# Kernel optimization log

Measured on AMD Instinct MI355X. Metric: run time of the kernel, lower is better.

## Reference

```python
import jax, jax.numpy as jnp
import numpy as np
from jax import lax

B, MIN, DIN = 16, 8, 16
MOUT, DOUT = 8, 16
H, W = 32, 32
K, S, P, OP = 3, 2, 1, 1
NH, NW = 64, 64
ITERS = 2
EPS = 1e-7


def squash(s):
    # s: [..., D]; matches torch squash: factor * s / safe_norm
    sq = jnp.sum(s * s, axis=-1, keepdims=True)
    norm = jnp.sqrt(sq + EPS)
    return (sq / (1.0 + sq)) * s / norm


def setup_inputs() -> dict:
    key = jax.random.key(0)
    k1, k2, k3 = jax.random.split(key, 3)
    x = jax.random.normal(k1, (B, MIN, H, W, DIN), dtype=jnp.float32)
    # torch ConvTranspose2d weight layout: [in_ch, out_ch, kH, kW]
    w_deconv = jax.random.normal(k2, (MIN * DIN, MOUT * DOUT, K, K), dtype=jnp.float32) * 0.05
    b_deconv = jax.random.normal(k3, (MOUT * DOUT,), dtype=jnp.float32) * 0.05
    b_route = jnp.zeros((1, MOUT, NH, NW, MIN), dtype=jnp.float32)
    return {"x": x, "w_deconv": w_deconv, "b_deconv": b_deconv, "b_route": b_route}


def reference(x, w_deconv, b_deconv, b_route):
    Bb, Min, Hh, Ww, Din = x.shape
    # [B, Min, H, W, Din] -> [B, Min*Din, H, W]
    xc = jnp.transpose(x, (0, 1, 4, 2, 3)).reshape(Bb, Min * Din, Hh, Ww)
    # ConvTranspose2d == conv with lhs_dilation=stride and spatially-flipped, IO-swapped kernel
    wf = jnp.transpose(w_deconv, (1, 0, 2, 3))[:, :, ::-1, ::-1]  # [out, in, kH, kW]
    pad = (K - 1 - P, K - 1 - P + OP)
    y = lax.conv_general_dilated(
        xc, wf, window_strides=(1, 1), padding=[pad, pad],
        lhs_dilation=(S, S), dimension_numbers=("NCHW", "OIHW", "NCHW"))
    y = y + b_deconv[None, :, None, None]  # [B, Mout*Dout, NH, NW]
    nh, nw = y.shape[2], y.shape[3]
    # view([B, Mout, Dout, h, w, -1]).permute(0,1,3,4,5,2) -> [B, Mout, h, w, 1, Dout]
    pred = jnp.transpose(y.reshape(Bb, MOUT, DOUT, nh, nw, 1), (0, 1, 3, 4, 5, 2))
    # --- agreement routing ---
    c = jax.nn.softmax(b_route, axis=-1)                      # [1, Mout, h, w, Min]
    out = squash(jnp.sum(c[..., None] * pred, axis=-2))       # [B, Mout, h, w, Dout]
    b = b_route
    for _ in range(ITERS):
        b = b + jnp.sum(pred * out[..., None, :], axis=-1)    # [B, Mout, h, w, Min]
        c = jax.nn.softmax(b, axis=-1)
        out = squash(jnp.sum(pred * c[..., None], axis=-2))
    return out
```

## Files before the change

kernel.cpp:

```cpp
#include <hip/hip_runtime.h>
#include <hip/hip_bf16.h>
#include <math.h>


typedef __attribute__((ext_vector_type(8))) __bf16 bf16x8;
typedef __attribute__((ext_vector_type(4))) float f32x4;

#define XBF_ELEMS (16 * 8 * 32 * 32 * 16)

__global__ __launch_bounds__(256) void prep(const float* __restrict__ x,
                                            const float* __restrict__ w,
                                            __hip_bfloat16* __restrict__ xbf,
                                            __hip_bfloat16* __restrict__ wl) {
    const int bx = blockIdx.x;
    if (bx < 1024) {
        const int i = (bx * 256 + threadIdx.x) * 8;
        float4 a = *(const float4*)(x + i);
        float4 b = *(const float4*)(x + i + 4);
        union { bf16x8 v; __hip_bfloat162 h[4]; } u;
        u.h[0] = __float22bfloat162_rn(make_float2(a.x, a.y));
        u.h[1] = __float22bfloat162_rn(make_float2(a.z, a.w));
        u.h[2] = __float22bfloat162_rn(make_float2(b.x, b.y));
        u.h[3] = __float22bfloat162_rn(make_float2(b.z, b.w));
        *(bf16x8*)(xbf + i) = u.v;
    } else {
        const int idx = (bx - 1024) * 256 + threadIdx.x;
        const int ci  = idx / 1152;
        const int rem = idx - ci * 1152;
        const int co  = rem / 9;
        const int tap = rem - co * 9;
        const int s = ci >> 5, quad = (ci >> 3) & 3, j = ci & 7;
        const int t = co >> 4, n16 = co & 15;
        const int dst = ((((tap * 4 + s) * 8 + t) * 64) + quad * 16 + n16) * 8 + j;
        wl[dst] = __float2bfloat16(w[idx]);
    }
}

template <int CTRL>
__device__ __forceinline__ float dpp_xadd(float v) {
    int p = __builtin_amdgcn_update_dpp(0, __float_as_int(v), CTRL, 0xF, 0xF, true);
    return v + __int_as_float(p);
}
__device__ __forceinline__ float rowsum16(float v) {
    v = dpp_xadd<0xB1>(v);
    v = dpp_xadd<0x4E>(v);
    v = dpp_xadd<0x141>(v);
    v = dpp_xadd<0x140>(v);
    return v;
}

template <int PH, int PW, int NT>
__device__ __forceinline__ void caps_body(
    const __hip_bfloat16* __restrict__ xbf, const __hip_bfloat16* __restrict__ wl,
    const float* __restrict__ bias, float* __restrict__ out,
    __hip_bfloat16* bsh, int t0)
{
    constexpr int NH = PH ? 2 : 1, NW = PW ? 2 : 1;
    constexpr int CHE = NT * 512;
    const int tid = threadIdx.x, lane = tid & 63, wv = tid >> 6;
    const int q = blockIdx.y, b = blockIdx.z;

    #pragma unroll
    for (int it = 0; it < 8; ++it) {
        const int idx    = it * 2048 + tid * 8;
        const int c2     = idx / CHE;
        const int within = idx % CHE;
        const int s  = c2 & 3, ti = c2 >> 2;
        const int kh = PH ? (ti / NW) * 2 : 1;
        const int kw = PW ? (ti % NW) * 2 : 1;
        const int tap = kh * 3 + kw;
        *(bf16x8*)(bsh + idx) =
            *(const bf16x8*)(wl + ((tap * 4 + s) * 8 + t0) * 512 + within);
    }
    __syncthreads();

    const int rp = wv >> 1, chf = wv & 1;
    const int rw0 = q * 4 + rp * 2;
    const int n16  = lane & 15;
    const int quad = lane >> 4;
    const int c    = chf * 16 + n16;

    float bb[NT];
    #pragma unroll
    for (int tt = 0; tt < NT; ++tt) bb[tt] = bias[(t0 + tt) * 16 + n16];

    const __hip_bfloat16* xq = xbf + b * 131072 + (quad >> 1) * 16384 + (quad & 1) * 8;

    f32x4 acc[2][NT];
    #pragma unroll
    for (int r = 0; r < 2; ++r)
        #pragma unroll
        for (int tt = 0; tt < NT; ++tt) acc[r][tt] = (f32x4){0.f, 0.f, 0.f, 0.f};

    #pragma unroll
    for (int khi = 0; khi < NH; ++khi) {
        const int dh = PH ? (1 - khi) : 0;
        const int ih0 = rw0 + dh, ih1 = ih0 + 1;
        const bool v0 = (ih0 < 32), v1 = (ih1 < 32);
        const int ih0c = v0 ? ih0 : 31, ih1c = v1 ? ih1 : 31;
        #pragma unroll
        for (int kwi = 0; kwi < NW; ++kwi) {
            const int dw = PW ? (1 - kwi) : 0;
            const int iw = c + dw;
            const bool vw = (iw < 32);
            const int iwc = vw ? iw : 31;
            const int ti = khi * NW + kwi;
            const __hip_bfloat16* a0p = xq + ih0c * 512 + iwc * 16;
            const __hip_bfloat16* a1p = xq + ih1c * 512 + iwc * 16;
            const __hip_bfloat16* wb  = bsh + ti * (4 * CHE) + lane * 8;
            #pragma unroll
            for (int s = 0; s < 4; ++s) {
                bf16x8 a0 = *(const bf16x8*)(a0p + s * 32768);
                bf16x8 a1 = *(const bf16x8*)(a1p + s * 32768);
                if (!(v0 && vw)) a0 = (bf16x8){};
                if (!(v1 && vw)) a1 = (bf16x8){};
                #pragma unroll
                for (int tt = 0; tt < NT; ++tt) {
                    bf16x8 bf = *(const bf16x8*)(wb + s * CHE + tt * 512);
                    acc[0][tt] = __builtin_amdgcn_mfma_f32_16x16x32_bf16(a0, bf, acc[0][tt], 0, 0, 0);
                    acc[1][tt] = __builtin_amdgcn_mfma_f32_16x16x32_bf16(a1, bf, acc[1][tt], 0, 0, 0);
                }
            }
        }
    }

    #pragma unroll
    for (int row = 0; row < 2; ++row) {
        const int oh = (rw0 + row) * 2 + PH;
        #pragma unroll
        for (int tt = 0; tt < NT; ++tt) {
            #pragma unroll
            for (int r = 0; r < 4; ++r) {
                const float y  = acc[row][tt][r] + bb[tt];
                const float s2 = rowsum16(y * y);
                const float f  = s2 / ((1.f + s2) * sqrtf(s2 + 1e-7f));
                const int ow = (chf * 16 + quad * 4 + r) * 2 + PW;
                __builtin_nontemporal_store(
                    y * f,
                    out + (((b * 8 + t0 + tt) * 64 + oh) * 64 + ow) * 16 + n16);
            }
        }
    }
}

__global__ __launch_bounds__(256, 4) void caps_mfma(
    const __hip_bfloat16* __restrict__ xbf, const __hip_bfloat16* __restrict__ wl,
    const float* __restrict__ bias, float* __restrict__ out)
{
    __shared__ __hip_bfloat16 bsh[16384];
    const int bx = blockIdx.x;
    if      (bx == 0) caps_body<0, 0, 8>(xbf, wl, bias, out, bsh, 0);
    else if (bx <  3) caps_body<0, 1, 4>(xbf, wl, bias, out, bsh, (bx - 1) * 4);
    else if (bx <  5) caps_body<1, 0, 4>(xbf, wl, bias, out, bsh, (bx - 3) * 4);
    else              caps_body<1, 1, 2>(xbf, wl, bias, out, bsh, (bx - 5) * 2);
}

extern "C" void kernel_launch(void* const* d_in, const int* in_sizes, int n_in,
                              void* d_out, int out_size, void* d_ws, size_t ws_size,
                              hipStream_t stream) {
    const float* x    = (const float*)d_in[0];
    const float* wgt  = (const float*)d_in[1];
    const float* bias = (const float*)d_in[2];
    float* out = (float*)d_out;

    __hip_bfloat16* xbf = (__hip_bfloat16*)d_ws;
    __hip_bfloat16* wlb = xbf + XBF_ELEMS;

    prep<<<1024 + 576, 256, 0, stream>>>(x, wgt, xbf, wlb);
    caps_mfma<<<dim3(9, 8, 16), 256, 0, stream>>>(xbf, wlb, bias, out);
}
```

Before: 93.00 us.

## Zero-pad bf16 input to 33x33, drop bounds checks, rebalance tap blocks

The prep kernel now writes the bf16 input into a zero-padded 33x33 spatial layout, so the MFMA kernel no longer clamps indices or masks out-of-range loads. The inner loop is restructured to load all four A fragments first and then issue the MFMAs, which gives the scheduler more independent loads to overlap. The (0,0) parity class is split into two blocks of NT=4 instead of one NT=8 block, making the grid 10 wide and balancing work across blocks. In exchange, prep writes slightly more data and does extra index arithmetic.

```diff
diff --git a/kernel.cpp b/kernel.cpp
--- a/kernel.cpp
+++ b/kernel.cpp
@@ -6,25 +6,41 @@
 typedef __attribute__((ext_vector_type(8))) __bf16 bf16x8;
 typedef __attribute__((ext_vector_type(4))) float f32x4;
 
-#define XBF_ELEMS (16 * 8 * 32 * 32 * 16)
+#define XPAD_ELEMS (16 * 8 * 33 * 33 * 16)
+#define XPAD_B 139392
+#define XPAD_MI 17424
+#define XPAD_IH 528
 
 __global__ __launch_bounds__(256) void prep(const float* __restrict__ x,
                                             const float* __restrict__ w,
                                             __hip_bfloat16* __restrict__ xbf,
                                             __hip_bfloat16* __restrict__ wl) {
     const int bx = blockIdx.x;
-    if (bx < 1024) {
-        const int i = (bx * 256 + threadIdx.x) * 8;
-        float4 a = *(const float4*)(x + i);
-        float4 b = *(const float4*)(x + i + 4);
-        union { bf16x8 v; __hip_bfloat162 h[4]; } u;
-        u.h[0] = __float22bfloat162_rn(make_float2(a.x, a.y));
-        u.h[1] = __float22bfloat162_rn(make_float2(a.z, a.w));
-        u.h[2] = __float22bfloat162_rn(make_float2(b.x, b.y));
-        u.h[3] = __float22bfloat162_rn(make_float2(b.z, b.w));
-        *(bf16x8*)(xbf + i) = u.v;
+    if (bx < 1089) {
+        const int i  = (bx * 256 + threadIdx.x) * 8;
+        const int b  = i / XPAD_B;
+        const int r1 = i - b * XPAD_B;
+        const int mi = r1 / XPAD_MI;
+        const int r2 = r1 - mi * XPAD_MI;
+        const int ih = r2 / XPAD_IH;
+        const int r3 = r2 - ih * XPAD_IH;
+        const int iw = r3 >> 4;
+        const int di = r3 & 15;
+        bf16x8 o = {};
+        if (ih < 32 && iw < 32) {
+            const float* s = x + b * 131072 + mi * 16384 + ih * 512 + iw * 16 + di;
+            float4 a = *(const float4*)s;
+            float4 c = *(const float4*)(s + 4);
+            union { bf16x8 v; __hip_bfloat162 h[4]; } u;
+            u.h[0] = __float22bfloat162_rn(make_float2(a.x, a.y));
+            u.h[1] = __float22bfloat162_rn(make_float2(a.z, a.w));
+            u.h[2] = __float22bfloat162_rn(make_float2(c.x, c.y));
+            u.h[3] = __float22bfloat162_rn(make_float2(c.z, c.w));
+            o = u.v;
+        }
+        *(bf16x8*)(xbf + i) = o;
     } else {
-        const int idx = (bx - 1024) * 256 + threadIdx.x;
+        const int idx = (bx - 1089) * 256 + threadIdx.x;
         const int ci  = idx / 1152;
         const int rem = idx - ci * 1152;
         const int co  = rem / 9;
@@ -56,12 +72,14 @@
     __hip_bfloat16* bsh, int t0)
 {
     constexpr int NH = PH ? 2 : 1, NW = PW ? 2 : 1;
-    constexpr int CHE = NT * 512;
+    constexpr int NTAP = NH * NW;
+    constexpr int CHE  = NT * 512;
+    constexpr int STG  = NTAP * 4 * CHE;
     const int tid = threadIdx.x, lane = tid & 63, wv = tid >> 6;
     const int q = blockIdx.y, b = blockIdx.z;
 
     #pragma unroll
-    for (int it = 0; it < 8; ++it) {
+    for (int it = 0; it < STG / 2048; ++it) {
         const int idx    = it * 2048 + tid * 8;
         const int c2     = idx / CHE;
         const int within = idx % CHE;
@@ -84,7 +102,7 @@
     #pragma unroll
     for (int tt = 0; tt < NT; ++tt) bb[tt] = bias[(t0 + tt) * 16 + n16];
 
-    const __hip_bfloat16* xq = xbf + b * 131072 + (quad >> 1) * 16384 + (quad & 1) * 8;
+    const __hip_bfloat16* xq = xbf + b * XPAD_B + (quad >> 1) * XPAD_MI + (quad & 1) * 8;
 
     f32x4 acc[2][NT];
     #pragma unroll
@@ -94,31 +112,28 @@
 
     #pragma unroll
     for (int khi = 0; khi < NH; ++khi) {
-        const int dh = PH ? (1 - khi) : 0;
-        const int ih0 = rw0 + dh, ih1 = ih0 + 1;
-        const bool v0 = (ih0 < 32), v1 = (ih1 < 32);
-        const int ih0c = v0 ? ih0 : 31, ih1c = v1 ? ih1 : 31;
+        const int dh  = PH ? (1 - khi) : 0;
+        const int ih0 = rw0 + dh;
         #pragma unroll
         for (int kwi = 0; kwi < NW; ++kwi) {
             const int dw = PW ? (1 - kwi) : 0;
             const int iw = c + dw;
-            const bool vw = (iw < 32);
-            const int iwc = vw ? iw : 31;
             const int ti = khi * NW + kwi;
-            const __hip_bfloat16* a0p = xq + ih0c * 512 + iwc * 16;
-            const __hip_bfloat16* a1p = xq + ih1c * 512 + iwc * 16;
-            const __hip_bfloat16* wb  = bsh + ti * (4 * CHE) + lane * 8;
+            const __hip_bfloat16* ap = xq + ih0 * XPAD_IH + iw * 16;
+            const __hip_bfloat16* wb = bsh + ti * (4 * CHE) + lane * 8;
+            bf16x8 a0[4], a1[4];
             #pragma unroll
             for (int s = 0; s < 4; ++s) {
-                bf16x8 a0 = *(const bf16x8*)(a0p + s * 32768);
-                bf16x8 a1 = *(const bf16x8*)(a1p + s * 32768);
-                if (!(v0 && vw)) a0 = (bf16x8){};
-                if (!(v1 && vw)) a1 = (bf16x8){};
+                a0[s] = *(const bf16x8*)(ap + s * (2 * XPAD_MI));
+                a1[s] = *(const bf16x8*)(ap + s * (2 * XPAD_MI) + XPAD_IH);
+            }
+            #pragma unroll
+            for (int tt = 0; tt < NT; ++tt) {
                 #pragma unroll
-                for (int tt = 0; tt < NT; ++tt) {
+                for (int s = 0; s < 4; ++s) {
                     bf16x8 bf = *(const bf16x8*)(wb + s * CHE + tt * 512);
-                    acc[0][tt] = __builtin_amdgcn_mfma_f32_16x16x32_bf16(a0, bf, acc[0][tt], 0, 0, 0);
-                    acc[1][tt] = __builtin_amdgcn_mfma_f32_16x16x32_bf16(a1, bf, acc[1][tt], 0, 0, 0);
+                    acc[0][tt] = __builtin_amdgcn_mfma_f32_16x16x32_bf16(a0[s], bf, acc[0][tt], 0, 0, 0);
+                    acc[1][tt] = __builtin_amdgcn_mfma_f32_16x16x32_bf16(a1[s], bf, acc[1][tt], 0, 0, 0);
                 }
             }
         }
@@ -149,10 +164,10 @@
 {
     __shared__ __hip_bfloat16 bsh[16384];
     const int bx = blockIdx.x;
-    if      (bx == 0) caps_body<0, 0, 8>(xbf, wl, bias, out, bsh, 0);
-    else if (bx <  3) caps_body<0, 1, 4>(xbf, wl, bias, out, bsh, (bx - 1) * 4);
-    else if (bx <  5) caps_body<1, 0, 4>(xbf, wl, bias, out, bsh, (bx - 3) * 4);
-    else              caps_body<1, 1, 2>(xbf, wl, bias, out, bsh, (bx - 5) * 2);
+    if      (bx <  2) caps_body<0, 0, 4>(xbf, wl, bias, out, bsh, bx * 4);
+    else if (bx <  4) caps_body<0, 1, 4>(xbf, wl, bias, out, bsh, (bx - 2) * 4);
+    else if (bx <  6) caps_body<1, 0, 4>(xbf, wl, bias, out, bsh, (bx - 4) * 4);
+    else              caps_body<1, 1, 2>(xbf, wl, bias, out, bsh, (bx - 6) * 2);
 }
 
 extern "C" void kernel_launch(void* const* d_in, const int* in_sizes, int n_in,
@@ -164,8 +179,8 @@
     float* out = (float*)d_out;
 
     __hip_bfloat16* xbf = (__hip_bfloat16*)d_ws;
-    __hip_bfloat16* wlb = xbf + XBF_ELEMS;
+    __hip_bfloat16* wlb = xbf + XPAD_ELEMS;
 
-    prep<<<1024 + 576, 256, 0, stream>>>(x, wgt, xbf, wlb);
-    caps_mfma<<<dim3(9, 8, 16), 256, 0, stream>>>(xbf, wlb, bias, out);
+    prep<<<1089 + 576, 256, 0, stream>>>(x, wgt, xbf, wlb);
+    caps_mfma<<<dim3(10, 8, 16), 256, 0, stream>>>(xbf, wlb, bias, out);
 }
```

New measurement: 91.29 us. Within noise of the previous version (-1.8%).
